# Optimization experiments

Hardware: AMD Instinct MI355X
Metric: run time of the kernel (lower is better)

The kernel has to match this reference:

```python
import jax, jax.numpy as jnp
import numpy as np

Q, N, K, F_IN, F_OUT = 4, 50000, 8, 128, 64


def setup_inputs() -> dict:
    key = jax.random.key(0)
    ks = jax.random.split(key, 5)
    query = jax.random.normal(ks[0], (Q, N, F_IN), dtype=jnp.float32)
    values = jax.random.normal(ks[1], (Q, N, F_IN), dtype=jnp.float32)
    edges = jax.random.randint(ks[2], (N, K), 0, N)  # neighbor index table
    W1 = jax.random.normal(ks[3], (F_IN, F_OUT), dtype=jnp.float32) / np.sqrt(F_IN).astype(np.float32)
    b1 = jnp.zeros((F_OUT,), jnp.float32)
    W2 = jax.random.normal(ks[4], (F_OUT, 1), dtype=jnp.float32) / np.sqrt(F_OUT).astype(np.float32)
    b2 = jnp.zeros((1,), jnp.float32)
    return {"query": query, "values": values, "edges": edges,
            "W1": W1, "b1": b1, "W2": W2, "b2": b2}


def _graph_conv(x, edges, W, b):
    # GraphConv: gather neighbor features via edge index table, mean-aggregate, linear.
    agg = x[edges].mean(axis=1)  # [N, K, F] -> [N, F]
    return agg @ W + b


def reference(query, values, edges, W1, b1, W2, b2):
    # Original loops over queries in Python; vectorize with vmap over Q.
    def per_query(q):  # q: [N, F_IN]
        h = jnp.tanh(_graph_conv(q, edges, W1, b1))  # [N, F_OUT]
        return _graph_conv(h, edges, W2, b2)         # [N, 1]

    score = jax.vmap(per_query)(query)               # [Q, N, 1]
    attention_weights = jax.nn.softmax(score, axis=1)
    context_vector = jnp.sum(attention_weights * values, axis=1)  # [Q, F_IN]
    return context_vector, score
```

## Files before the change

### kernel.cpp

```cpp
#include <hip/hip_runtime.h>
#include <hip/hip_fp16.h>
#include <math.h>


#define FIN 128
#define FOUT 64
#define KN 8
#define CTXB 250

typedef _Float16 f16x8 __attribute__((ext_vector_type(8)));
typedef float f32x4 __attribute__((ext_vector_type(4)));

__global__ __launch_bounds__(256, 3) void k_xw(const float* __restrict__ query,
                                               const float* __restrict__ W1,
                                               __half* __restrict__ y, int N) {
    __shared__ _Float16 Wlds[8192];
    const int tid = threadIdx.x;
    #pragma unroll
    for (int it = 0; it < 4; ++it) {
        int p = it * 256 + tid;
        int g6 = p >> 6;
        int kk = g6 >> 2, nt = g6 & 3;
        int lane6 = p & 63;
        int lg = lane6 >> 4, lr = lane6 & 15;
        int f = nt * 16 + lr;
        int kbase = kk * 32 + lg * 8;
        f16x8 fr;
        #pragma unroll
        for (int j = 0; j < 8; ++j)
            fr[j] = (_Float16)W1[(kbase + j) * FOUT + f];
        ((f16x8*)Wlds)[p] = fr;
    }
    __syncthreads();

    const int wave = tid >> 6, lane = tid & 63;
    const int lg = lane >> 4, lr = lane & 15;
    const int q = blockIdx.y;
    const int base = blockIdx.x * 128 + wave * 32;
    const float* qb = query + (size_t)q * N * FIN;
    __half* yq = y + (size_t)q * N * FOUT;
    const f16x8* Bp = (const f16x8*)Wlds;

    int n0 = base + lr;       if (n0 >= N) n0 = N - 1;
    int n1 = base + 16 + lr;  if (n1 >= N) n1 = N - 1;
    const float4* r0 = (const float4*)(qb + (size_t)n0 * FIN);
    const float4* r1 = (const float4*)(qb + (size_t)n1 * FIN);

    float4 a0[8], a1[8];
    #pragma unroll
    for (int kk = 0; kk < 4; ++kk) {
        a0[2 * kk]     = r0[kk * 8 + lg * 2];
        a0[2 * kk + 1] = r0[kk * 8 + lg * 2 + 1];
        a1[2 * kk]     = r1[kk * 8 + lg * 2];
        a1[2 * kk + 1] = r1[kk * 8 + lg * 2 + 1];
    }

    f32x4 acc0[4], acc1[4];
    #pragma unroll
    for (int nt = 0; nt < 4; ++nt) { acc0[nt] = (f32x4)0.f; acc1[nt] = (f32x4)0.f; }

    #pragma unroll
    for (int kk = 0; kk < 4; ++kk) {
        f16x8 A0, A1;
        const float* x0 = (const float*)&a0[2 * kk];
        const float* x1 = (const float*)&a1[2 * kk];
        #pragma unroll
        for (int j = 0; j < 8; ++j) { A0[j] = (_Float16)x0[j]; A1[j] = (_Float16)x1[j]; }
        #pragma unroll
        for (int nt = 0; nt < 4; ++nt) {
            f16x8 Bf = Bp[(kk * 4 + nt) * 64 + lane];
            acc0[nt] = __builtin_amdgcn_mfma_f32_16x16x32_f16(A0, Bf, acc0[nt], 0, 0, 0);
            acc1[nt] = __builtin_amdgcn_mfma_f32_16x16x32_f16(A1, Bf, acc1[nt], 0, 0, 0);
        }
    }
    #pragma unroll
    for (int r = 0; r < 4; ++r) {
        int m0 = base + lg * 4 + r;
        int m1 = base + 16 + lg * 4 + r;
        if (m0 < N) {
            #pragma unroll
            for (int nt = 0; nt < 4; ++nt)
                yq[(size_t)m0 * FOUT + nt * 16 + lr] = __float2half(acc0[nt][r]);
        }
        if (m1 < N) {
            #pragma unroll
            for (int nt = 0; nt < 4; ++nt)
                yq[(size_t)m1 * FOUT + nt * 16 + lr] = __float2half(acc1[nt][r]);
        }
    }
}

__global__ __launch_bounds__(256, 4) void k_agg(const __half* __restrict__ y,
                                                const int* __restrict__ edges,
                                                const float* __restrict__ b1,
                                                const float* __restrict__ W2,
                                                float* __restrict__ s1, int N) {
    const int tid = threadIdx.x;
    const int wave = tid >> 6, lane = tid & 63;
    const int half = lane >> 5, fl = lane & 31;
    const int q = blockIdx.y;
    const int nA = blockIdx.x * 16 + wave * 2 + half;
    const int nB = nA + 8;
    const int ncA = nA < N ? nA : N - 1;
    const int ncB = nB < N ? nB : N - 1;
    const __half2* y2 = (const __half2*)(y + (size_t)q * N * FOUT);

    const int4* erA = (const int4*)(edges + (size_t)ncA * KN);
    const int4* erB = (const int4*)(edges + (size_t)ncB * KN);
    int4 eaA = erA[0], ebA = erA[1];
    int4 eaB = erB[0], ebB = erB[1];

    __half2 a0 = y2[(size_t)eaA.x * 32 + fl], a1 = y2[(size_t)eaA.y * 32 + fl];
    __half2 a2 = y2[(size_t)eaA.z * 32 + fl], a3 = y2[(size_t)eaA.w * 32 + fl];
    __half2 a4 = y2[(size_t)ebA.x * 32 + fl], a5 = y2[(size_t)ebA.y * 32 + fl];
    __half2 a6 = y2[(size_t)ebA.z * 32 + fl], a7 = y2[(size_t)ebA.w * 32 + fl];
    __half2 c0 = y2[(size_t)eaB.x * 32 + fl], c1 = y2[(size_t)eaB.y * 32 + fl];
    __half2 c2 = y2[(size_t)eaB.z * 32 + fl], c3 = y2[(size_t)eaB.w * 32 + fl];
    __half2 c4 = y2[(size_t)ebB.x * 32 + fl], c5 = y2[(size_t)ebB.y * 32 + fl];
    __half2 c6 = y2[(size_t)ebB.z * 32 + fl], c7 = y2[(size_t)ebB.w * 32 + fl];

    __half2 sA = __hadd2(__hadd2(__hadd2(a0, a1), __hadd2(a2, a3)),
                         __hadd2(__hadd2(a4, a5), __hadd2(a6, a7)));
    __half2 sB = __hadd2(__hadd2(__hadd2(c0, c1), __hadd2(c2, c3)),
                         __hadd2(__hadd2(c4, c5), __hadd2(c6, c7)));
    float2 fA = __half22float2(sA);
    float2 fB = __half22float2(sB);

    float2 bv = *(const float2*)(b1 + fl * 2);
    float2 wv = *(const float2*)(W2 + fl * 2);

    float xA0 = fA.x * 0.125f + bv.x, xA1 = fA.y * 0.125f + bv.y;
    float xB0 = fB.x * 0.125f + bv.x, xB1 = fB.y * 0.125f + bv.y;
    float eA0 = __expf(-2.f * fabsf(xA0)), eA1 = __expf(-2.f * fabsf(xA1));
    float eB0 = __expf(-2.f * fabsf(xB0)), eB1 = __expf(-2.f * fabsf(xB1));
    float tA0 = copysignf(__fdividef(1.f - eA0, 1.f + eA0), xA0);
    float tA1 = copysignf(__fdividef(1.f - eA1, 1.f + eA1), xA1);
    float tB0 = copysignf(__fdividef(1.f - eB0, 1.f + eB0), xB0);
    float tB1 = copysignf(__fdividef(1.f - eB1, 1.f + eB1), xB1);
    float pA = tA0 * wv.x + tA1 * wv.y;
    float pB = tB0 * wv.x + tB1 * wv.y;
    #pragma unroll
    for (int off = 16; off; off >>= 1) {
        pA += __shfl_xor(pA, off);
        pB += __shfl_xor(pB, off);
    }
    if (fl == 0) {
        float* s1q = s1 + (size_t)q * N;
        if (nA < N) s1q[nA] = pA;
        if (nB < N) s1q[nB] = pB;
    }
}

__global__ __launch_bounds__(256, 4) void k_ctx(const float* __restrict__ values,
                                                const float* __restrict__ s1,
                                                const int* __restrict__ edges,
                                                const float* __restrict__ b2,
                                                float* __restrict__ score,
                                                float* __restrict__ partial,
                                                float* __restrict__ zpart, int N) {
    const int q = blockIdx.y, cb = blockIdx.x;
    const int tid = threadIdx.x;
    const int chunk = (N + CTXB - 1) / CTXB;
    const int n0 = cb * chunk, n1 = min(n0 + chunk, N);
    const int cnt = n1 - n0;
    __shared__ float wlds[256];
    __shared__ float zred[4];
    const float* s1q = s1 + (size_t)q * N;
    const float b2v = b2[0];

    float zp = 0.f;
    if (tid < cnt) {
        int n = n0 + tid;
        float acc = 0.f;
        #pragma unroll
        for (int k = 0; k < KN; ++k) acc += s1q[edges[(size_t)n * KN + k]];
        float sc = acc * 0.125f + b2v;
        score[(size_t)q * N + n] = sc;
        float ex = __expf(sc);
        wlds[tid] = ex;
        zp = ex;
    }
    float z = zp;
    #pragma unroll
    for (int off = 32; off; off >>= 1) z += __shfl_xor(z, off);
    if ((tid & 63) == 0) zred[tid >> 6] = z;
    __syncthreads();

    const int fi = tid & 31, g = tid >> 5;
    const float4* v = (const float4*)(values + (size_t)q * N * FIN);
    float4 acc = make_float4(0.f, 0.f, 0.f, 0.f);
    int n = n0 + g;
    for (; n + 56 < n1; n += 64) {
        int l = n - n0;
        float w0 = wlds[l],      w1 = wlds[l + 8],  w2 = wlds[l + 16], w3 = wlds[l + 24];
        float w4 = wlds[l + 32], w5 = wlds[l + 40], w6 = wlds[l + 48], w7 = wlds[l + 56];
        float4 v0 = v[(size_t)n * 32 + fi];
        float4 v1 = v[(size_t)(n + 8) * 32 + fi];
        float4 v2 = v[(size_t)(n + 16) * 32 + fi];
        float4 v3 = v[(size_t)(n + 24) * 32 + fi];
        float4 v4 = v[(size_t)(n + 32) * 32 + fi];
        float4 v5 = v[(size_t)(n + 40) * 32 + fi];
        float4 v6 = v[(size_t)(n + 48) * 32 + fi];
        float4 v7 = v[(size_t)(n + 56) * 32 + fi];
        acc.x = fmaf(w0, v0.x, acc.x); acc.y = fmaf(w0, v0.y, acc.y);
        acc.z = fmaf(w0, v0.z, acc.z); acc.w = fmaf(w0, v0.w, acc.w);
        acc.x = fmaf(w1, v1.x, acc.x); acc.y = fmaf(w1, v1.y, acc.y);
        acc.z = fmaf(w1, v1.z, acc.z); acc.w = fmaf(w1, v1.w, acc.w);
        acc.x = fmaf(w2, v2.x, acc.x); acc.y = fmaf(w2, v2.y, acc.y);
        acc.z = fmaf(w2, v2.z, acc.z); acc.w = fmaf(w2, v2.w, acc.w);
        acc.x = fmaf(w3, v3.x, acc.x); acc.y = fmaf(w3, v3.y, acc.y);
        acc.z = fmaf(w3, v3.z, acc.z); acc.w = fmaf(w3, v3.w, acc.w);
        acc.x = fmaf(w4, v4.x, acc.x); acc.y = fmaf(w4, v4.y, acc.y);
        acc.z = fmaf(w4, v4.z, acc.z); acc.w = fmaf(w4, v4.w, acc.w);
        acc.x = fmaf(w5, v5.x, acc.x); acc.y = fmaf(w5, v5.y, acc.y);
        acc.z = fmaf(w5, v5.z, acc.z); acc.w = fmaf(w5, v5.w, acc.w);
        acc.x = fmaf(w6, v6.x, acc.x); acc.y = fmaf(w6, v6.y, acc.y);
        acc.z = fmaf(w6, v6.z, acc.z); acc.w = fmaf(w6, v6.w, acc.w);
        acc.x = fmaf(w7, v7.x, acc.x); acc.y = fmaf(w7, v7.y, acc.y);
        acc.z = fmaf(w7, v7.z, acc.z); acc.w = fmaf(w7, v7.w, acc.w);
    }
    for (; n < n1; n += 8) {
        float ww = wlds[n - n0];
        float4 a = v[(size_t)n * 32 + fi];
        acc.x = fmaf(ww, a.x, acc.x);
        acc.y = fmaf(ww, a.y, acc.y);
        acc.z = fmaf(ww, a.z, acc.z);
        acc.w = fmaf(ww, a.w, acc.w);
    }
    __shared__ float4 part[256];
    part[tid] = acc;
    __syncthreads();
    if (tid < 32) {
        float4 a = part[tid];
        #pragma unroll
        for (int gg = 1; gg < 8; ++gg) {
            float4 b = part[gg * 32 + tid];
            a.x += b.x; a.y += b.y; a.z += b.z; a.w += b.w;
        }
        ((float4*)partial)[((size_t)q * CTXB + cb) * 32 + fi] = a;
    }
    if (tid == 0) zpart[(size_t)q * CTXB + cb] = zred[0] + zred[1] + zred[2] + zred[3];
}

__global__ __launch_bounds__(512) void k_final(const float* __restrict__ partial,
                                               const float* __restrict__ zpart,
                                               float* __restrict__ ctx) {
    const int q = blockIdx.x;
    const int tid = threadIdx.x;
    const int f = tid & 127, h = tid >> 7;
    const float* p = partial + (size_t)q * CTXB * FIN;
    float s = 0.f;
    for (int b = h; b < CTXB; b += 4) s += p[(size_t)b * FIN + f];
    __shared__ float red[512];
    __shared__ float zred[8];
    red[tid] = s;
    float z = (tid < CTXB) ? zpart[(size_t)q * CTXB + tid] : 0.f;
    #pragma unroll
    for (int off = 32; off; off >>= 1) z += __shfl_xor(z, off);
    if ((tid & 63) == 0) zred[tid >> 6] = z;
    __syncthreads();
    if (tid < 128) {
        float Zt = zred[0] + zred[1] + zred[2] + zred[3] +
                   zred[4] + zred[5] + zred[6] + zred[7];
        float t = red[tid] + red[tid + 128] + red[tid + 256] + red[tid + 384];
        ctx[q * FIN + f] = t * (1.f / Zt);
    }
}

extern "C" void kernel_launch(void* const* d_in, const int* in_sizes, int n_in,
                              void* d_out, int out_size, void* d_ws, size_t ws_size,
                              hipStream_t stream) {
    const float* query  = (const float*)d_in[0];
    const float* values = (const float*)d_in[1];
    const int*   edges  = (const int*)d_in[2];
    const float* W1     = (const float*)d_in[3];
    const float* b1     = (const float*)d_in[4];
    const float* W2     = (const float*)d_in[5];
    const float* b2     = (const float*)d_in[6];

    const int N = in_sizes[2] / KN;
    const int Q = in_sizes[0] / (N * FIN);

    float* out   = (float*)d_out;
    float* ctx   = out;
    float* score = out + (size_t)Q * FIN;

    char* ws = (char*)d_ws;
    __half* y = (__half*)ws;
    size_t off = (size_t)Q * N * FOUT * sizeof(__half);
    float* s1    = (float*)(ws + off);  off += (size_t)Q * N * sizeof(float);
    float* part  = (float*)(ws + off);  off += (size_t)Q * CTXB * FIN * sizeof(float);
    float* zpart = (float*)(ws + off);

    dim3 g1((N + 127) / 128, Q);
    k_xw<<<g1, 256, 0, stream>>>(query, W1, y, N);
    dim3 g2((N + 15) / 16, Q);
    k_agg<<<g2, 256, 0, stream>>>(y, edges, b1, W2, s1, N);
    dim3 g3(CTXB, Q);
    k_ctx<<<g3, 256, 0, stream>>>(values, s1, edges, b2, score, part, zpart, N);
    k_final<<<Q, 512, 0, stream>>>(part, zpart, ctx);
}
```

Before: 87.47 us.

## Fuse four pipeline kernels into one cooperative persistent kernel with grid syncs

Replaces the four separate launches (projection, neighbor aggregation, context partials, final reduce) with a single cooperative persistent kernel of 512 blocks. Phases are separated by grid-wide barriers, and each phase loops over its work units. This removes launch gaps between kernels and the per-kernel ramp-up and tail. In exchange it pays for grid.sync barriers, lower occupancy, and a projection phase that handles 16 rows per wave instead of 32. The old multi-kernel path is kept as a fallback if the cooperative launch fails.

```diff
diff --git a/kernel.cpp b/kernel.cpp
--- a/kernel.cpp
+++ b/kernel.cpp
@@ -1,15 +1,256 @@
 #include <hip/hip_runtime.h>
 #include <hip/hip_fp16.h>
+#include <hip/hip_cooperative_groups.h>
 #include <math.h>
+
+namespace cg = cooperative_groups;
 
 
 #define FIN 128
 #define FOUT 64
 #define KN 8
 #define CTXB 250
+#define CHUNK 200
+#define GRID 512
 
 typedef _Float16 f16x8 __attribute__((ext_vector_type(8)));
 typedef float f32x4 __attribute__((ext_vector_type(4)));
+
+__global__ __launch_bounds__(256, 2) void k_mega(
+        const float* __restrict__ query, const float* __restrict__ values,
+        const int* __restrict__ edges, const float* __restrict__ W1,
+        const float* __restrict__ b1, const float* __restrict__ W2,
+        const float* __restrict__ b2, float* __restrict__ ctx,
+        float* __restrict__ score, __half* __restrict__ y,
+        float* __restrict__ s1, float* __restrict__ partial,
+        float* __restrict__ zpart, int N, int Q) {
+    cg::grid_group grid = cg::this_grid();
+    __shared__ _Float16 Wlds[8192];
+    __shared__ float wlds[256];
+    __shared__ float zred[4];
+    __shared__ float4 part[256];
+    __shared__ float red2[256];
+
+    const int tid = threadIdx.x;
+    const int bid = blockIdx.x;
+    const int nBlocks = gridDim.x;
+    const int wave = tid >> 6, lane = tid & 63;
+    const int lg = lane >> 4, lr = lane & 15;
+    const int unitsPerQ = (N + 15) / 16;
+    const int totalUnits = unitsPerQ * Q;
+
+    #pragma unroll
+    for (int it = 0; it < 4; ++it) {
+        int p = it * 256 + tid;
+        int g6 = p >> 6;
+        int kk = g6 >> 2, nt = g6 & 3;
+        int lane6 = p & 63;
+        int plg = lane6 >> 4, plr = lane6 & 15;
+        int f = nt * 16 + plr;
+        int kbase = kk * 32 + plg * 8;
+        f16x8 fr;
+        #pragma unroll
+        for (int j = 0; j < 8; ++j)
+            fr[j] = (_Float16)W1[(kbase + j) * FOUT + f];
+        ((f16x8*)Wlds)[p] = fr;
+    }
+    __syncthreads();
+    const f16x8* Bp = (const f16x8*)Wlds;
+
+    for (int u = bid * 4 + wave; u < totalUnits; u += nBlocks * 4) {
+        int q = u / unitsPerQ, t = u % unitsPerQ;
+        int base = t * 16;
+        const float* qb = query + (size_t)q * N * FIN;
+        __half* yq = y + (size_t)q * N * FOUT;
+        int n0 = base + lr; if (n0 >= N) n0 = N - 1;
+        const float4* r0 = (const float4*)(qb + (size_t)n0 * FIN);
+        float4 a0[8];
+        #pragma unroll
+        for (int kk = 0; kk < 4; ++kk) {
+            a0[2 * kk]     = r0[kk * 8 + lg * 2];
+            a0[2 * kk + 1] = r0[kk * 8 + lg * 2 + 1];
+        }
+        f32x4 acc[4];
+        #pragma unroll
+        for (int nt = 0; nt < 4; ++nt) acc[nt] = (f32x4)0.f;
+        #pragma unroll
+        for (int kk = 0; kk < 4; ++kk) {
+            f16x8 A0;
+            const float* x0 = (const float*)&a0[2 * kk];
+            #pragma unroll
+            for (int j = 0; j < 8; ++j) A0[j] = (_Float16)x0[j];
+            #pragma unroll
+            for (int nt = 0; nt < 4; ++nt) {
+                f16x8 Bf = Bp[(kk * 4 + nt) * 64 + lane];
+                acc[nt] = __builtin_amdgcn_mfma_f32_16x16x32_f16(A0, Bf, acc[nt], 0, 0, 0);
+            }
+        }
+        #pragma unroll
+        for (int r = 0; r < 4; ++r) {
+            int m0 = base + lg * 4 + r;
+            if (m0 < N) {
+                #pragma unroll
+                for (int nt = 0; nt < 4; ++nt)
+                    yq[(size_t)m0 * FOUT + nt * 16 + lr] = __float2half(acc[nt][r]);
+            }
+        }
+    }
+    grid.sync();
+
+    {
+        const int half = lane >> 5, fl = lane & 31;
+        for (int u = bid; u < totalUnits; u += nBlocks) {
+            int q = u / unitsPerQ, t = u % unitsPerQ;
+            int nA = t * 16 + wave * 2 + half;
+            int nB = nA + 8;
+            int ncA = nA < N ? nA : N - 1;
+            int ncB = nB < N ? nB : N - 1;
+            const __half2* y2 = (const __half2*)(y + (size_t)q * N * FOUT);
+            const int4* erA = (const int4*)(edges + (size_t)ncA * KN);
+            const int4* erB = (const int4*)(edges + (size_t)ncB * KN);
+            int4 eaA = erA[0], ebA = erA[1];
+            int4 eaB = erB[0], ebB = erB[1];
+
+            __half2 a0 = y2[(size_t)eaA.x * 32 + fl], a1 = y2[(size_t)eaA.y * 32 + fl];
+            __half2 a2 = y2[(size_t)eaA.z * 32 + fl], a3 = y2[(size_t)eaA.w * 32 + fl];
+            __half2 a4 = y2[(size_t)ebA.x * 32 + fl], a5 = y2[(size_t)ebA.y * 32 + fl];
+            __half2 a6 = y2[(size_t)ebA.z * 32 + fl], a7 = y2[(size_t)ebA.w * 32 + fl];
+            __half2 c0 = y2[(size_t)eaB.x * 32 + fl], c1 = y2[(size_t)eaB.y * 32 + fl];
+            __half2 c2 = y2[(size_t)eaB.z * 32 + fl], c3 = y2[(size_t)eaB.w * 32 + fl];
+            __half2 c4 = y2[(size_t)ebB.x * 32 + fl], c5 = y2[(size_t)ebB.y * 32 + fl];
+            __half2 c6 = y2[(size_t)ebB.z * 32 + fl], c7 = y2[(size_t)ebB.w * 32 + fl];
+
+            __half2 sA = __hadd2(__hadd2(__hadd2(a0, a1), __hadd2(a2, a3)),
+                                 __hadd2(__hadd2(a4, a5), __hadd2(a6, a7)));
+            __half2 sB = __hadd2(__hadd2(__hadd2(c0, c1), __hadd2(c2, c3)),
+                                 __hadd2(__hadd2(c4, c5), __hadd2(c6, c7)));
+            float2 fA = __half22float2(sA);
+            float2 fB = __half22float2(sB);
+            float2 bv = *(const float2*)(b1 + fl * 2);
+            float2 wv = *(const float2*)(W2 + fl * 2);
+            float xA0 = fA.x * 0.125f + bv.x, xA1 = fA.y * 0.125f + bv.y;
+            float xB0 = fB.x * 0.125f + bv.x, xB1 = fB.y * 0.125f + bv.y;
+            float eA0 = __expf(-2.f * fabsf(xA0)), eA1 = __expf(-2.f * fabsf(xA1));
+            float eB0 = __expf(-2.f * fabsf(xB0)), eB1 = __expf(-2.f * fabsf(xB1));
+            float tA0 = copysignf(__fdividef(1.f - eA0, 1.f + eA0), xA0);
+            float tA1 = copysignf(__fdividef(1.f - eA1, 1.f + eA1), xA1);
+            float tB0 = copysignf(__fdividef(1.f - eB0, 1.f + eB0), xB0);
+            float tB1 = copysignf(__fdividef(1.f - eB1, 1.f + eB1), xB1);
+            float pA = tA0 * wv.x + tA1 * wv.y;
+            float pB = tB0 * wv.x + tB1 * wv.y;
+            #pragma unroll
+            for (int off = 16; off; off >>= 1) {
+                pA += __shfl_xor(pA, off);
+                pB += __shfl_xor(pB, off);
+            }
+            if (fl == 0) {
+                float* s1q = s1 + (size_t)q * N;
+                if (nA < N) s1q[nA] = pA;
+                if (nB < N) s1q[nB] = pB;
+            }
+        }
+    }
+    grid.sync();
+
+    for (int c = bid; c < CTXB * Q; c += nBlocks) {
+        const int q = c / CTXB, cb = c % CTXB;
+        const int n0 = cb * CHUNK, n1 = min(n0 + CHUNK, N);
+        const int cnt = n1 - n0;
+        const float* s1q = s1 + (size_t)q * N;
+        const float b2v = b2[0];
+
+        float zp = 0.f;
+        if (tid < cnt) {
+            int n = n0 + tid;
+            float acc = 0.f;
+            #pragma unroll
+            for (int k = 0; k < KN; ++k) acc += s1q[edges[(size_t)n * KN + k]];
+            float sc = acc * 0.125f + b2v;
+            score[(size_t)q * N + n] = sc;
+            float ex = __expf(sc);
+            wlds[tid] = ex;
+            zp = ex;
+        }
+        float z = zp;
+        #pragma unroll
+        for (int off = 32; off; off >>= 1) z += __shfl_xor(z, off);
+        if ((tid & 63) == 0) zred[tid >> 6] = z;
+        __syncthreads();
+
+        const int fi = tid & 31, g = tid >> 5;
+        const float4* v = (const float4*)(values + (size_t)q * N * FIN);
+        float4 acc = make_float4(0.f, 0.f, 0.f, 0.f);
+        int n = n0 + g;
+        for (; n + 56 < n1; n += 64) {
+            int l = n - n0;
+            float w0 = wlds[l],      w1 = wlds[l + 8],  w2 = wlds[l + 16], w3 = wlds[l + 24];
+            float w4 = wlds[l + 32], w5 = wlds[l + 40], w6 = wlds[l + 48], w7 = wlds[l + 56];
+            float4 v0 = v[(size_t)n * 32 + fi];
+            float4 v1 = v[(size_t)(n + 8) * 32 + fi];
+            float4 v2 = v[(size_t)(n + 16) * 32 + fi];
+            float4 v3 = v[(size_t)(n + 24) * 32 + fi];
+            float4 v4 = v[(size_t)(n + 32) * 32 + fi];
+            float4 v5 = v[(size_t)(n + 40) * 32 + fi];
+            float4 v6 = v[(size_t)(n + 48) * 32 + fi];
+            float4 v7 = v[(size_t)(n + 56) * 32 + fi];
+            acc.x = fmaf(w0, v0.x, acc.x); acc.y = fmaf(w0, v0.y, acc.y);
+            acc.z = fmaf(w0, v0.z, acc.z); acc.w = fmaf(w0, v0.w, acc.w);
+            acc.x = fmaf(w1, v1.x, acc.x); acc.y = fmaf(w1, v1.y, acc.y);
+            acc.z = fmaf(w1, v1.z, acc.z); acc.w = fmaf(w1, v1.w, acc.w);
+            acc.x = fmaf(w2, v2.x, acc.x); acc.y = fmaf(w2, v2.y, acc.y);
+            acc.z = fmaf(w2, v2.z, acc.z); acc.w = fmaf(w2, v2.w, acc.w);
+            acc.x = fmaf(w3, v3.x, acc.x); acc.y = fmaf(w3, v3.y, acc.y);
+            acc.z = fmaf(w3, v3.z, acc.z); acc.w = fmaf(w3, v3.w, acc.w);
+            acc.x = fmaf(w4, v4.x, acc.x); acc.y = fmaf(w4, v4.y, acc.y);
+            acc.z = fmaf(w4, v4.z, acc.z); acc.w = fmaf(w4, v4.w, acc.w);
+            acc.x = fmaf(w5, v5.x, acc.x); acc.y = fmaf(w5, v5.y, acc.y);
+            acc.z = fmaf(w5, v5.z, acc.z); acc.w = fmaf(w5, v5.w, acc.w);
+            acc.x = fmaf(w6, v6.x, acc.x); acc.y = fmaf(w6, v6.y, acc.y);
+            acc.z = fmaf(w6, v6.z, acc.z); acc.w = fmaf(w6, v6.w, acc.w);
+            acc.x = fmaf(w7, v7.x, acc.x); acc.y = fmaf(w7, v7.y, acc.y);
+            acc.z = fmaf(w7, v7.z, acc.z); acc.w = fmaf(w7, v7.w, acc.w);
+        }
+        for (; n < n1; n += 8) {
+            float ww = wlds[n - n0];
+            float4 a = v[(size_t)n * 32 + fi];
+            acc.x = fmaf(ww, a.x, acc.x);
+            acc.y = fmaf(ww, a.y, acc.y);
+            acc.z = fmaf(ww, a.z, acc.z);
+            acc.w = fmaf(ww, a.w, acc.w);
+        }
+        part[tid] = acc;
+        __syncthreads();
+        if (tid < 32) {
+            float4 a = part[tid];
+            #pragma unroll
+            for (int gg = 1; gg < 8; ++gg) {
+                float4 b = part[gg * 32 + tid];
+                a.x += b.x; a.y += b.y; a.z += b.z; a.w += b.w;
+            }
+            ((float4*)partial)[((size_t)q * CTXB + cb) * 32 + fi] = a;
+        }
+        if (tid == 0) zpart[(size_t)q * CTXB + cb] = zred[0] + zred[1] + zred[2] + zred[3];
+        __syncthreads();
+    }
+    grid.sync();
+
+    if (bid < Q) {
+        const float* p = partial + (size_t)bid * CTXB * FIN;
+        const int f = tid & 127, h = tid >> 7;
+        float s = 0.f;
+        for (int b = h; b < CTXB; b += 2) s += p[(size_t)b * FIN + f];
+        red2[tid] = s;
+        float z = (tid < CTXB) ? zpart[(size_t)bid * CTXB + tid] : 0.f;
+        #pragma unroll
+        for (int off = 32; off; off >>= 1) z += __shfl_xor(z, off);
+        if ((tid & 63) == 0) zred[tid >> 6] = z;
+        __syncthreads();
+        if (tid < 128) {
+            float Zt = zred[0] + zred[1] + zred[2] + zred[3];
+            ctx[bid * FIN + f] = (red2[tid] + red2[tid + 128]) * (1.f / Zt);
+        }
+    }
+}
 
 __global__ __launch_bounds__(256, 3) void k_xw(const float* __restrict__ query,
                                                const float* __restrict__ W1,
@@ -54,11 +295,9 @@
         a1[2 * kk]     = r1[kk * 8 + lg * 2];
         a1[2 * kk + 1] = r1[kk * 8 + lg * 2 + 1];
     }
-
     f32x4 acc0[4], acc1[4];
     #pragma unroll
     for (int nt = 0; nt < 4; ++nt) { acc0[nt] = (f32x4)0.f; acc1[nt] = (f32x4)0.f; }
-
     #pragma unroll
     for (int kk = 0; kk < 4; ++kk) {
         f16x8 A0, A1;
@@ -125,10 +364,8 @@
                          __hadd2(__hadd2(c4, c5), __hadd2(c6, c7)));
     float2 fA = __half22float2(sA);
     float2 fB = __half22float2(sB);
-
     float2 bv = *(const float2*)(b1 + fl * 2);
     float2 wv = *(const float2*)(W2 + fl * 2);
-
     float xA0 = fA.x * 0.125f + bv.x, xA1 = fA.y * 0.125f + bv.y;
     float xB0 = fB.x * 0.125f + bv.x, xB1 = fB.y * 0.125f + bv.y;
     float eA0 = __expf(-2.f * fabsf(xA0)), eA1 = __expf(-2.f * fabsf(xA1));
@@ -160,8 +397,7 @@
                                                 float* __restrict__ zpart, int N) {
     const int q = blockIdx.y, cb = blockIdx.x;
     const int tid = threadIdx.x;
-    const int chunk = (N + CTXB - 1) / CTXB;
-    const int n0 = cb * chunk, n1 = min(n0 + chunk, N);
+    const int n0 = cb * CHUNK, n1 = min(n0 + CHUNK, N);
     const int cnt = n1 - n0;
     __shared__ float wlds[256];
     __shared__ float zred[4];
@@ -278,8 +514,8 @@
     const float* W2     = (const float*)d_in[5];
     const float* b2     = (const float*)d_in[6];
 
-    const int N = in_sizes[2] / KN;
-    const int Q = in_sizes[0] / (N * FIN);
+    int N = in_sizes[2] / KN;
+    int Q = in_sizes[0] / (N * FIN);
 
     float* out   = (float*)d_out;
     float* ctx   = out;
@@ -292,11 +528,19 @@
     float* part  = (float*)(ws + off);  off += (size_t)Q * CTXB * FIN * sizeof(float);
     float* zpart = (float*)(ws + off);
 
-    dim3 g1((N + 127) / 128, Q);
-    k_xw<<<g1, 256, 0, stream>>>(query, W1, y, N);
-    dim3 g2((N + 15) / 16, Q);
-    k_agg<<<g2, 256, 0, stream>>>(y, edges, b1, W2, s1, N);
-    dim3 g3(CTXB, Q);
-    k_ctx<<<g3, 256, 0, stream>>>(values, s1, edges, b2, score, part, zpart, N);
-    k_final<<<Q, 512, 0, stream>>>(part, zpart, ctx);
+    void* args[] = {(void*)&query, (void*)&values, (void*)&edges, (void*)&W1,
+                    (void*)&b1, (void*)&W2, (void*)&b2, (void*)&ctx,
+                    (void*)&score, (void*)&y, (void*)&s1, (void*)&part,
+                    (void*)&zpart, (void*)&N, (void*)&Q};
+    hipError_t err = hipLaunchCooperativeKernel((void*)k_mega, dim3(GRID),
+                                                dim3(256), args, 0, stream);
+    if (err != hipSuccess) {
+        dim3 g1((N + 127) / 128, Q);
+        k_xw<<<g1, 256, 0, stream>>>(query, W1, y, N);
+        dim3 g2((N + 15) / 16, Q);
+        k_agg<<<g2, 256, 0, stream>>>(y, edges, b1, W2, s1, N);
+        dim3 g3(CTXB, Q);
+        k_ctx<<<g3, 256, 0, stream>>>(values, s1, edges, b2, score, part, zpart, N);
+        k_final<<<Q, 512, 0, stream>>>(part, zpart, ctx);
+    }
 }
```

Measured after the change: 299.2 us. +242.1%, slower.

## Fuse final context reduction into k_ctx via last-block atomic counter

Applied to the files above, without the earlier changes.

Removes the separate k_final launch by having each k_ctx block increment a per-query atomic counter, with the last block reducing all partial sums and normalizing. The counter is zeroed inside k_xw. The W1 staging into LDS is moved after the query loads are issued so they overlap. Chunk size is fixed at 200 rows, which covers N only if N <= 250*200. This saves a kernel launch and its tail, but adds a threadfence and an atomic per block and a serialized final reduction inside one block.

```diff
diff --git a/kernel.cpp b/kernel.cpp
--- a/kernel.cpp
+++ b/kernel.cpp
@@ -7,45 +7,31 @@
 #define FOUT 64
 #define KN 8
 #define CTXB 250
+#define CHUNK 200
 
 typedef _Float16 f16x8 __attribute__((ext_vector_type(8)));
 typedef float f32x4 __attribute__((ext_vector_type(4)));
 
 __global__ __launch_bounds__(256, 3) void k_xw(const float* __restrict__ query,
                                                const float* __restrict__ W1,
-                                               __half* __restrict__ y, int N) {
+                                               __half* __restrict__ y,
+                                               int* __restrict__ counter,
+                                               int N, int Q) {
     __shared__ _Float16 Wlds[8192];
     const int tid = threadIdx.x;
-    #pragma unroll
-    for (int it = 0; it < 4; ++it) {
-        int p = it * 256 + tid;
-        int g6 = p >> 6;
-        int kk = g6 >> 2, nt = g6 & 3;
-        int lane6 = p & 63;
-        int lg = lane6 >> 4, lr = lane6 & 15;
-        int f = nt * 16 + lr;
-        int kbase = kk * 32 + lg * 8;
-        f16x8 fr;
-        #pragma unroll
-        for (int j = 0; j < 8; ++j)
-            fr[j] = (_Float16)W1[(kbase + j) * FOUT + f];
-        ((f16x8*)Wlds)[p] = fr;
-    }
-    __syncthreads();
-
     const int wave = tid >> 6, lane = tid & 63;
     const int lg = lane >> 4, lr = lane & 15;
     const int q = blockIdx.y;
     const int base = blockIdx.x * 128 + wave * 32;
     const float* qb = query + (size_t)q * N * FIN;
     __half* yq = y + (size_t)q * N * FOUT;
-    const f16x8* Bp = (const f16x8*)Wlds;
+
+    if (blockIdx.x == 0 && blockIdx.y == 0 && tid < Q) counter[tid] = 0;
 
     int n0 = base + lr;       if (n0 >= N) n0 = N - 1;
     int n1 = base + 16 + lr;  if (n1 >= N) n1 = N - 1;
     const float4* r0 = (const float4*)(qb + (size_t)n0 * FIN);
     const float4* r1 = (const float4*)(qb + (size_t)n1 * FIN);
-
     float4 a0[8], a1[8];
     #pragma unroll
     for (int kk = 0; kk < 4; ++kk) {
@@ -54,6 +40,24 @@
         a1[2 * kk]     = r1[kk * 8 + lg * 2];
         a1[2 * kk + 1] = r1[kk * 8 + lg * 2 + 1];
     }
+
+    #pragma unroll
+    for (int it = 0; it < 4; ++it) {
+        int p = it * 256 + tid;
+        int g6 = p >> 6;
+        int kk = g6 >> 2, nt = g6 & 3;
+        int lane6 = p & 63;
+        int plg = lane6 >> 4, plr = lane6 & 15;
+        int f = nt * 16 + plr;
+        int kbase = kk * 32 + plg * 8;
+        f16x8 fr;
+        #pragma unroll
+        for (int j = 0; j < 8; ++j)
+            fr[j] = (_Float16)W1[(kbase + j) * FOUT + f];
+        ((f16x8*)Wlds)[p] = fr;
+    }
+    __syncthreads();
+    const f16x8* Bp = (const f16x8*)Wlds;
 
     f32x4 acc0[4], acc1[4];
     #pragma unroll
@@ -128,7 +132,6 @@
 
     float2 bv = *(const float2*)(b1 + fl * 2);
     float2 wv = *(const float2*)(W2 + fl * 2);
-
     float xA0 = fA.x * 0.125f + bv.x, xA1 = fA.y * 0.125f + bv.y;
     float xB0 = fB.x * 0.125f + bv.x, xB1 = fB.y * 0.125f + bv.y;
     float eA0 = __expf(-2.f * fabsf(xA0)), eA1 = __expf(-2.f * fabsf(xA1));
@@ -157,14 +160,18 @@
                                                 const float* __restrict__ b2,
                                                 float* __restrict__ score,
                                                 float* __restrict__ partial,
-                                                float* __restrict__ zpart, int N) {
+                                                float* __restrict__ zpart,
+                                                int* __restrict__ counter,
+                                                float* __restrict__ ctx, int N) {
     const int q = blockIdx.y, cb = blockIdx.x;
     const int tid = threadIdx.x;
-    const int chunk = (N + CTXB - 1) / CTXB;
-    const int n0 = cb * chunk, n1 = min(n0 + chunk, N);
+    const int n0 = cb * CHUNK, n1 = min(n0 + CHUNK, N);
     const int cnt = n1 - n0;
     __shared__ float wlds[256];
     __shared__ float zred[4];
+    __shared__ float4 part[256];
+    __shared__ float red2[256];
+    __shared__ int isLast;
     const float* s1q = s1 + (size_t)q * N;
     const float b2v = b2[0];
 
@@ -227,7 +234,6 @@
         acc.z = fmaf(ww, a.z, acc.z);
         acc.w = fmaf(ww, a.w, acc.w);
     }
-    __shared__ float4 part[256];
     part[tid] = acc;
     __syncthreads();
     if (tid < 32) {
@@ -240,30 +246,29 @@
         ((float4*)partial)[((size_t)q * CTXB + cb) * 32 + fi] = a;
     }
     if (tid == 0) zpart[(size_t)q * CTXB + cb] = zred[0] + zred[1] + zred[2] + zred[3];
-}
-
-__global__ __launch_bounds__(512) void k_final(const float* __restrict__ partial,
-                                               const float* __restrict__ zpart,
-                                               float* __restrict__ ctx) {
-    const int q = blockIdx.x;
-    const int tid = threadIdx.x;
-    const int f = tid & 127, h = tid >> 7;
-    const float* p = partial + (size_t)q * CTXB * FIN;
-    float s = 0.f;
-    for (int b = h; b < CTXB; b += 4) s += p[(size_t)b * FIN + f];
-    __shared__ float red[512];
-    __shared__ float zred[8];
-    red[tid] = s;
-    float z = (tid < CTXB) ? zpart[(size_t)q * CTXB + tid] : 0.f;
-    #pragma unroll
-    for (int off = 32; off; off >>= 1) z += __shfl_xor(z, off);
-    if ((tid & 63) == 0) zred[tid >> 6] = z;
-    __syncthreads();
-    if (tid < 128) {
-        float Zt = zred[0] + zred[1] + zred[2] + zred[3] +
-                   zred[4] + zred[5] + zred[6] + zred[7];
-        float t = red[tid] + red[tid + 128] + red[tid + 256] + red[tid + 384];
-        ctx[q * FIN + f] = t * (1.f / Zt);
+
+    __threadfence();
+    __syncthreads();
+    if (tid == 0) {
+        int old = atomicAdd(&counter[q], 1);
+        isLast = (old == CTXB - 1);
+    }
+    __syncthreads();
+    if (isLast) {
+        const float* p = partial + (size_t)q * CTXB * FIN;
+        const int f = tid & 127, h = tid >> 7;
+        float s = 0.f;
+        for (int b = h; b < CTXB; b += 2) s += p[(size_t)b * FIN + f];
+        red2[tid] = s;
+        float zz = (tid < CTXB) ? zpart[(size_t)q * CTXB + tid] : 0.f;
+        #pragma unroll
+        for (int off = 32; off; off >>= 1) zz += __shfl_xor(zz, off);
+        if ((tid & 63) == 0) zred[tid >> 6] = zz;
+        __syncthreads();
+        if (tid < 128) {
+            float Zt = zred[0] + zred[1] + zred[2] + zred[3];
+            ctx[q * FIN + f] = (red2[tid] + red2[tid + 128]) * (1.f / Zt);
+        }
     }
 }
 
@@ -278,8 +283,8 @@
     const float* W2     = (const float*)d_in[5];
     const float* b2     = (const float*)d_in[6];
 
-    const int N = in_sizes[2] / KN;
-    const int Q = in_sizes[0] / (N * FIN);
+    int N = in_sizes[2] / KN;
+    int Q = in_sizes[0] / (N * FIN);
 
     float* out   = (float*)d_out;
     float* ctx   = out;
@@ -290,13 +295,14 @@
     size_t off = (size_t)Q * N * FOUT * sizeof(__half);
     float* s1    = (float*)(ws + off);  off += (size_t)Q * N * sizeof(float);
     float* part  = (float*)(ws + off);  off += (size_t)Q * CTXB * FIN * sizeof(float);
-    float* zpart = (float*)(ws + off);
+    float* zpart = (float*)(ws + off);  off += (size_t)Q * CTXB * sizeof(float);
+    int* counter = (int*)(ws + off);
 
     dim3 g1((N + 127) / 128, Q);
-    k_xw<<<g1, 256, 0, stream>>>(query, W1, y, N);
+    k_xw<<<g1, 256, 0, stream>>>(query, W1, y, counter, N, Q);
     dim3 g2((N + 15) / 16, Q);
     k_agg<<<g2, 256, 0, stream>>>(y, edges, b1, W2, s1, N);
     dim3 g3(CTXB, Q);
-    k_ctx<<<g3, 256, 0, stream>>>(values, s1, edges, b2, score, part, zpart, N);
-    k_final<<<Q, 512, 0, stream>>>(part, zpart, ctx);
+    k_ctx<<<g3, 256, 0, stream>>>(values, s1, edges, b2, score, part, zpart,
+                                  counter, ctx, N);
 }
```

Result: slower. 207.3 us (+137.0%).
